# Optimization experiments

Measured on AMD Instinct MI355X. Metric: run time of the kernel, lower is better.

## Reference

```python
import jax, jax.numpy as jnp
import numpy as np

DIM = 2048
N_HEADS = 16
Q_LORA = 1536
KV_LORA = 512
NOPE = 128
ROPE = 64
V_DIM = 128
B, T = 1, 3072
EPS = 1e-6


def rmsnorm(x, w):
    var = jnp.mean(jnp.square(x), axis=-1, keepdims=True)
    return x * jax.lax.rsqrt(var + EPS) * w


def apply_rope(x, cos, sin):
    # x: (B, T, H, d); cos/sin: (T, d//2) -> broadcast (1, T, 1, d//2)
    c = cos[None, :, None, :]
    s = sin[None, :, None, :]
    x1 = x[..., 0::2]
    x2 = x[..., 1::2]
    r1 = x1 * c - x2 * s
    r2 = x1 * s + x2 * c
    return jnp.stack([r1, r2], axis=-1).reshape(x.shape)


def setup_inputs() -> dict:
    key = jax.random.key(0)
    ks = jax.random.split(key, 10)
    std = 0.02
    x = jax.random.normal(ks[0], (B, T, DIM), dtype=jnp.float32)
    # RoPE angles: position * inv_freq, shape (T, ROPE//2)
    inv_freq = 1.0 / (10000.0 ** (np.arange(0, ROPE, 2, dtype=np.float32) / ROPE))
    freqs = jnp.asarray(np.arange(T, dtype=np.float32)[:, None] * inv_freq[None, :])
    # additive causal mask (T, T)
    mask = jnp.where(jnp.tril(jnp.ones((T, T), dtype=bool)), 0.0, -jnp.inf).astype(jnp.float32)
    wq_down = jax.random.normal(ks[1], (DIM, Q_LORA), dtype=jnp.float32) * std
    q_norm_w = jnp.ones((Q_LORA,), dtype=jnp.float32)
    wq_nope = jax.random.normal(ks[2], (Q_LORA, N_HEADS * NOPE), dtype=jnp.float32) * std
    wq_rope = jax.random.normal(ks[3], (Q_LORA, N_HEADS * ROPE), dtype=jnp.float32) * std
    wkv_down = jax.random.normal(ks[4], (DIM, KV_LORA + ROPE), dtype=jnp.float32) * std
    kv_norm_w = jnp.ones((KV_LORA,), dtype=jnp.float32)
    wkv_up = jax.random.normal(ks[5], (KV_LORA, N_HEADS * (NOPE + V_DIM)), dtype=jnp.float32) * std
    wo = jax.random.normal(ks[6], (N_HEADS * V_DIM, DIM), dtype=jnp.float32) * std
    return {
        'x': x, 'freqs': freqs, 'mask': mask,
        'wq_down': wq_down, 'q_norm_w': q_norm_w, 'wq_nope': wq_nope,
        'wq_rope': wq_rope, 'wkv_down': wkv_down, 'kv_norm_w': kv_norm_w,
        'wkv_up': wkv_up, 'wo': wo,
    }


def reference(x, freqs, mask, wq_down, q_norm_w, wq_nope, wq_rope,
              wkv_down, kv_norm_w, wkv_up, wo):
    cos, sin = jnp.cos(freqs), jnp.sin(freqs)
    # Q path: down-project, RMSNorm, split nope/rope heads
    q_lat = rmsnorm(x @ wq_down, q_norm_w)                      # (B,T,Q_LORA)
    q_nope = (q_lat @ wq_nope).reshape(B, T, N_HEADS, NOPE)
    q_rope = apply_rope((q_lat @ wq_rope).reshape(B, T, N_HEADS, ROPE), cos, sin)
    q = jnp.concatenate([q_nope, q_rope], axis=-1)              # (B,T,H,192)
    # KV path: joint down-projection -> latent c_kv + raw rope key
    kvd = x @ wkv_down                                          # (B,T,KV_LORA+ROPE)
    c_kv = kvd[..., :KV_LORA]
    k_rope_raw = kvd[..., KV_LORA:]                             # (B,T,ROPE)
    k_rope = jnp.broadcast_to(k_rope_raw[:, :, None, :], (B, T, N_HEADS, ROPE))
    k_rope = apply_rope(k_rope, cos, sin)
    kv_up = (rmsnorm(c_kv, kv_norm_w) @ wkv_up).reshape(B, T, N_HEADS, NOPE + V_DIM)
    k_nope = kv_up[..., :NOPE]
    v = kv_up[..., NOPE:]                                       # (B,T,H,V_DIM)
    k = jnp.concatenate([k_nope, k_rope], axis=-1)              # (B,T,H,192)
    scale = (NOPE + ROPE) ** (-0.5)
    attn = jnp.einsum('bqhd,bkhd->bhqk', q, k) * scale + mask[None, None]
    attn = jax.nn.softmax(attn, axis=-1)                        # dropout p=0 (eval)
    out = jnp.einsum('bhqk,bkhd->bqhd', attn, v).reshape(B, T, N_HEADS * V_DIM)
    return out @ wo                                             # (B,T,DIM)
```

## Files before the change

kernel.cpp:

```cpp
#include <hip/hip_runtime.h>
#include <hip/hip_bf16.h>

typedef __bf16 bf16_t;
typedef __bf16 bf16x8 __attribute__((ext_vector_type(8)));
typedef float f32x4 __attribute__((ext_vector_type(4)));

#define T_SEQ 3072
#define DIM 2048
#define NH 16
#define QLORA 1536
#define KVLORA 512
#define NOPE 128
#define ROPE 64
#define VDIM 128
#define HD 192
#define SCALE 0.07216878364870323f
#define CHUNK 12

__device__ inline float wave_reduce_sum(float v) {
    #pragma unroll
    for (int off = 32; off > 0; off >>= 1) v += __shfl_down(v, off);
    return v;
}

__device__ inline float block_reduce_sum_256(float v) {
    __shared__ float red[4];
    int lane = threadIdx.x & 63, w = threadIdx.x >> 6;
    v = wave_reduce_sum(v);
    if (lane == 0) red[w] = v;
    __syncthreads();
    if (threadIdx.x == 0) red[0] = red[0] + red[1] + red[2] + red[3];
    __syncthreads();
    return red[0];
}

__device__ inline void glds16(const bf16_t* g, bf16_t* l) {
    __builtin_amdgcn_global_load_lds(
        (const __attribute__((address_space(1))) unsigned int*)g,
        (__attribute__((address_space(3))) unsigned int*)l, 16, 0, 0);
}

__global__ void f2b_kernel(const float* __restrict__ in, bf16_t* __restrict__ out, int n) {
    int i = (blockIdx.x * 256 + threadIdx.x) * 4;
    if (i < n) {
        float4 v = *(const float4*)&in[i];
        bf16_t o[4] = {(bf16_t)v.x, (bf16_t)v.y, (bf16_t)v.z, (bf16_t)v.w};
        *(uint2*)&out[i] = *(const uint2*)o;
    }
}

__global__ __launch_bounds__(256) void transp_kernel(
    const float* __restrict__ in, bf16_t* __restrict__ out, int K, int N)
{
    __shared__ float tile[32][33];
    int k0 = blockIdx.y * 32, n0 = blockIdx.x * 32;
    int tx = threadIdx.x & 31, ty = threadIdx.x >> 5;
    #pragma unroll
    for (int i = 0; i < 4; ++i)
        tile[ty + i * 8][tx] = in[(size_t)(k0 + ty + i * 8) * N + n0 + tx];
    __syncthreads();
    #pragma unroll
    for (int i = 0; i < 4; ++i)
        out[(size_t)(n0 + ty + i * 8) * K + k0 + tx] = (bf16_t)tile[tx][ty + i * 8];
}

__global__ __launch_bounds__(256) void vt_transp(
    const bf16_t* __restrict__ kvu, bf16_t* __restrict__ vt)
{
    __shared__ bf16_t tile[32][34];
    int t0 = blockIdx.x * 32, d0 = blockIdx.y * 32, h = blockIdx.z;
    int tx = threadIdx.x & 31, ty = threadIdx.x >> 5;
    #pragma unroll
    for (int i = 0; i < 4; ++i)
        tile[ty + i * 8][tx] = kvu[(size_t)(t0 + ty + i * 8) * (NH * 256) + h * 256 + NOPE + d0 + tx];
    __syncthreads();
    #pragma unroll
    for (int i = 0; i < 4; ++i)
        vt[((size_t)h * VDIM + d0 + ty + i * 8) * T_SEQ + t0 + tx] = tile[tx][ty + i * 8];
}

__global__ __launch_bounds__(256) void gemm_mfma(
    const bf16_t* __restrict__ A, const bf16_t* __restrict__ Bt,
    float* __restrict__ Cf, bf16_t* __restrict__ Cb,
    int M, int N, int K, int writef)
{
    __shared__ __align__(16) bf16_t As[128 * 32];
    __shared__ __align__(16) bf16_t Bs[128 * 32];
    int tid = threadIdx.x;
    int w = tid >> 6, lane = tid & 63;
    int quad = lane >> 4, l16 = lane & 15;
    int bm = blockIdx.y * 128, bn = blockIdx.x * 128;
    int wm = (w & 1) * 64, wn = (w >> 1) * 64;

    int srow = tid >> 2, soff = (tid & 3) * 8;
    const bf16_t* a0 = A + (size_t)(bm + srow) * K + soff;
    const bf16_t* a1 = A + (size_t)(bm + 64 + srow) * K + soff;
    int br0 = bn + srow;      if (br0 >= N) br0 = N - 1;
    int br1 = bn + 64 + srow; if (br1 >= N) br1 = N - 1;
    const bf16_t* b0 = Bt + (size_t)br0 * K + soff;
    const bf16_t* b1 = Bt + (size_t)br1 * K + soff;
    bf16_t* la = &As[tid * 8];
    bf16_t* lb = &Bs[tid * 8];

    f32x4 acc[4][4];
    #pragma unroll
    for (int i = 0; i < 4; ++i)
        #pragma unroll
        for (int j = 0; j < 4; ++j)
            acc[i][j] = (f32x4){0.f, 0.f, 0.f, 0.f};

    for (int k0 = 0; k0 < K; k0 += 32) {
        glds16(a0 + k0, la);
        glds16(a1 + k0, la + 2048);
        glds16(b0 + k0, lb);
        glds16(b1 + k0, lb + 2048);
        __syncthreads();
        bf16x8 af[4], bfr[4];
        #pragma unroll
        for (int t = 0; t < 4; ++t) {
            af[t]  = *(const bf16x8*)&As[(wm + t * 16 + l16) * 32 + quad * 8];
            bfr[t] = *(const bf16x8*)&Bs[(wn + t * 16 + l16) * 32 + quad * 8];
        }
        #pragma unroll
        for (int i = 0; i < 4; ++i)
            #pragma unroll
            for (int j = 0; j < 4; ++j)
                acc[i][j] = __builtin_amdgcn_mfma_f32_16x16x32_bf16(af[i], bfr[j], acc[i][j], 0, 0, 0);
        __syncthreads();
    }

    #pragma unroll
    for (int i = 0; i < 4; ++i) {
        #pragma unroll
        for (int j = 0; j < 4; ++j) {
            #pragma unroll
            for (int r = 0; r < 4; ++r) {
                int row = bm + wm + i * 16 + quad * 4 + r;
                int col = bn + wn + j * 16 + l16;
                if (col < N) {
                    if (writef) Cf[(size_t)row * N + col] = acc[i][j][r];
                    else        Cb[(size_t)row * N + col] = (bf16_t)acc[i][j][r];
                }
            }
        }
    }
}

__global__ __launch_bounds__(256) void rmsnorm_rows(
    bf16_t* __restrict__ X, const float* __restrict__ w, int N)
{
    int row = blockIdx.x;
    bf16_t* x = X + (size_t)row * N;
    float ss = 0.f;
    for (int i = threadIdx.x; i < N; i += 256) { float v = (float)x[i]; ss += v * v; }
    ss = block_reduce_sum_256(ss);
    float sc = rsqrtf(ss / (float)N + 1e-6f);
    for (int i = threadIdx.x; i < N; i += 256)
        x[i] = (bf16_t)((float)x[i] * sc * w[i]);
}

__global__ __launch_bounds__(256) void kv_post(
    const bf16_t* __restrict__ kvd, const float* __restrict__ w,
    const float* __restrict__ freqs,
    bf16_t* __restrict__ ckvn, bf16_t* __restrict__ kr)
{
    int row = blockIdx.x;
    const bf16_t* src = kvd + (size_t)row * (KVLORA + ROPE);
    float ss = 0.f;
    for (int i = threadIdx.x; i < KVLORA; i += 256) { float v = (float)src[i]; ss += v * v; }
    ss = block_reduce_sum_256(ss);
    float sc = rsqrtf(ss / (float)KVLORA + 1e-6f);
    for (int i = threadIdx.x; i < KVLORA; i += 256)
        ckvn[(size_t)row * KVLORA + i] = (bf16_t)((float)src[i] * sc * w[i]);
    if (threadIdx.x < 32) {
        int i = threadIdx.x;
        float f = freqs[row * 32 + i];
        float c = cosf(f), s = sinf(f);
        float x1 = (float)src[KVLORA + 2 * i], x2 = (float)src[KVLORA + 2 * i + 1];
        kr[(size_t)row * ROPE + 2 * i]     = (bf16_t)(x1 * c - x2 * s);
        kr[(size_t)row * ROPE + 2 * i + 1] = (bf16_t)(x1 * s + x2 * c);
    }
}

__global__ void rope_q(bf16_t* __restrict__ qr, const float* __restrict__ freqs) {
    int idx = blockIdx.x * 256 + threadIdx.x;
    if (idx >= T_SEQ * NH * 32) return;
    int t = idx >> 9;
    int rem = idx & 511;
    int h = rem >> 5;
    int i = rem & 31;
    float f = freqs[t * 32 + i];
    float c = cosf(f), s = sinf(f);
    bf16_t* p = qr + (size_t)t * (NH * ROPE) + h * ROPE + 2 * i;
    float x1 = (float)p[0], x2 = (float)p[1];
    p[0] = (bf16_t)(x1 * c - x2 * s);
    p[1] = (bf16_t)(x1 * s + x2 * c);
}

#define P_STRIDE 72
__device__ inline int slot_base(int qt, int h) {
    int b = qt / CHUNK;
    return h * 120 + qt + 6 * b * (b - 1) + (qt - CHUNK * b) * b;
}
__global__ __launch_bounds__(256) void attn_v8(
    const bf16_t* __restrict__ QN, const bf16_t* __restrict__ QR,
    const bf16_t* __restrict__ KVU, const bf16_t* __restrict__ KR,
    const bf16_t* __restrict__ Vt,
    bf16_t* __restrict__ Opart, float* __restrict__ lpart)
{
    __shared__ __align__(16) bf16_t Kn[64 * 128];
    __shared__ __align__(16) bf16_t Kr[64 * 64];
    __shared__ __align__(16) bf16_t Vs[128 * 64];
    __shared__ __align__(16) bf16_t Ps[4][16 * P_STRIDE];

    int qt = blockIdx.x, cx = blockIdx.y, h = blockIdx.z;
    if (cx > qt / CHUNK) return;
    int slot = slot_base(qt, h) + cx;
    int kt0 = cx * CHUNK;
    int kt1 = min(qt + 1, kt0 + CHUNK);

    int tid = threadIdx.x;
    int w = tid >> 6, lane = tid & 63;
    int quad = lane >> 4, l16 = lane & 15;
    int qbase = qt * 64;

    bf16x8 qf[6];
    {
        int qrow = qbase + w * 16 + l16;
        #pragma unroll
        for (int kk = 0; kk < 4; ++kk)
            qf[kk] = *(const bf16x8*)&QN[(size_t)qrow * (NH * NOPE) + h * NOPE + kk * 32 + quad * 8];
        #pragma unroll
        for (int kk = 4; kk < 6; ++kk)
            qf[kk] = *(const bf16x8*)&QR[(size_t)qrow * (NH * ROPE) + h * ROPE + (kk - 4) * 32 + quad * 8];
    }

    int l4 = lane >> 4, l3 = lane >> 3;
    const bf16_t* kn_e = KVU + (size_t)(kt0 * 64 + w * 16 + l4) * (NH * 256) + h * 256 + ((lane & 15) ^ l4) * 8;
    const bf16_t* kn_o = KVU + (size_t)(kt0 * 64 + w * 16 + l4) * (NH * 256) + h * 256 + ((lane & 15) ^ (4 + l4)) * 8;
    const bf16_t* krp  = KR  + (size_t)(kt0 * 64 + w * 16 + l3) * ROPE + ((lane & 7) ^ l3) * 8;
    const bf16_t* vp   = Vt  + ((size_t)h * VDIM + w * 32 + l3) * T_SEQ + kt0 * 64 + ((lane & 7) ^ l3) * 8;

    bf16x8 ones;
    #pragma unroll
    for (int i = 0; i < 8; ++i) ones[i] = (bf16_t)1.0f;

    f32x4 o[8];
    #pragma unroll
    for (int nt = 0; nt < 8; ++nt) o[nt] = (f32x4){0.f, 0.f, 0.f, 0.f};
    f32x4 lacc = (f32x4){0.f, 0.f, 0.f, 0.f};

    for (int kt = kt0; kt < kt1; ++kt) {
        int kbase = kt * 64;
        #pragma unroll
        for (int i = 0; i < 4; ++i)
            glds16(((i & 1) ? kn_o : kn_e) + (size_t)i * 4 * (NH * 256), &Kn[(w * 4 + i) * 512]);
        #pragma unroll
        for (int i = 0; i < 2; ++i)
            glds16(krp + (size_t)i * 8 * ROPE, &Kr[(w * 2 + i) * 512]);
        #pragma unroll
        for (int i = 0; i < 4; ++i)
            glds16(vp + (size_t)i * 8 * T_SEQ, &Vs[(w * 4 + i) * 512]);
        kn_e += (size_t)64 * NH * 256;
        kn_o += (size_t)64 * NH * 256;
        krp  += 64 * ROPE;
        vp   += 64;
        __syncthreads();

        f32x4 S[4];
        #pragma unroll
        for (int c = 0; c < 4; ++c) S[c] = (f32x4){0.f, 0.f, 0.f, 0.f};
        #pragma unroll
        for (int kk = 0; kk < 4; ++kk) {
            #pragma unroll
            for (int c = 0; c < 4; ++c) {
                bf16x8 kf = *(const bf16x8*)&Kn[(c * 16 + l16) * 128 + (((kk * 4 + quad) ^ (l16 & 7)) * 8)];
                S[c] = __builtin_amdgcn_mfma_f32_16x16x32_bf16(qf[kk], kf, S[c], 0, 0, 0);
            }
        }
        #pragma unroll
        for (int kk = 4; kk < 6; ++kk) {
            #pragma unroll
            for (int c = 0; c < 4; ++c) {
                bf16x8 kf = *(const bf16x8*)&Kr[(c * 16 + l16) * 64 + ((((kk - 4) * 4 + quad) ^ (l16 & 7)) * 8)];
                S[c] = __builtin_amdgcn_mfma_f32_16x16x32_bf16(qf[kk], kf, S[c], 0, 0, 0);
            }
        }

        #pragma unroll
        for (int c = 0; c < 4; ++c) {
            #pragma unroll
            for (int j = 0; j < 4; ++j) {
                int col = kbase + c * 16 + l16;
                int grow = qbase + w * 16 + quad * 4 + j;
                float p = (col <= grow) ? __expf(S[c][j] * SCALE) : 0.f;
                Ps[w][(quad * 4 + j) * P_STRIDE + c * 16 + l16] = (bf16_t)p;
            }
        }
        __asm__ volatile("s_waitcnt lgkmcnt(0)" ::: "memory");

        bf16x8 pf0 = *(const bf16x8*)&Ps[w][l16 * P_STRIDE + quad * 8];
        bf16x8 pf1 = *(const bf16x8*)&Ps[w][l16 * P_STRIDE + 32 + quad * 8];
        lacc = __builtin_amdgcn_mfma_f32_16x16x32_bf16(pf0, ones, lacc, 0, 0, 0);
        lacc = __builtin_amdgcn_mfma_f32_16x16x32_bf16(pf1, ones, lacc, 0, 0, 0);

        #pragma unroll
        for (int kk2 = 0; kk2 < 2; ++kk2) {
            bf16x8 pf = kk2 ? pf1 : pf0;
            #pragma unroll
            for (int nt = 0; nt < 8; ++nt) {
                bf16x8 vf = *(const bf16x8*)&Vs[(nt * 16 + l16) * 64 + (((kk2 * 4 + quad) ^ (l16 & 7)) * 8)];
                o[nt] = __builtin_amdgcn_mfma_f32_16x16x32_bf16(pf, vf, o[nt], 0, 0, 0);
            }
        }
        __syncthreads();
    }

    #pragma unroll
    for (int nt = 0; nt < 8; ++nt)
        #pragma unroll
        for (int j = 0; j < 4; ++j)
            Opart[(size_t)slot * 8192 + (w * 16 + quad * 4 + j) * 128 + nt * 16 + l16] = (bf16_t)o[nt][j];
    if (l16 == 0) {
        #pragma unroll
        for (int j = 0; j < 4; ++j)
            lpart[slot * 64 + w * 16 + quad * 4 + j] = lacc[j];
    }
}

__global__ __launch_bounds__(256) void attn_combine(
    const bf16_t* __restrict__ Opart, const float* __restrict__ lpart,
    bf16_t* __restrict__ AO)
{
    int qt = blockIdx.x, h = blockIdx.y;
    int nch = qt / CHUNK + 1;
    int base = slot_base(qt, h);
    int r = threadIdx.x >> 2, c0 = (threadIdx.x & 3) * 32;

    float acc[32];
    #pragma unroll
    for (int i = 0; i < 32; ++i) acc[i] = 0.f;
    float lsum = 0.f;
    for (int ch = 0; ch < nch; ++ch) {
        int slot = base + ch;
        const bf16_t* p = &Opart[(size_t)slot * 8192 + r * 128 + c0];
        #pragma unroll
        for (int v = 0; v < 4; ++v) {
            bf16x8 u = *(const bf16x8*)&p[v * 8];
            #pragma unroll
            for (int e = 0; e < 8; ++e) acc[v * 8 + e] += (float)u[e];
        }
        lsum += lpart[slot * 64 + r];
    }
    float inv = 1.0f / lsum;
    bf16_t* dst = AO + (size_t)(qt * 64 + r) * (NH * VDIM) + h * VDIM + c0;
    #pragma unroll
    for (int v = 0; v < 4; ++v) {
        bf16_t tmp[8];
        #pragma unroll
        for (int e = 0; e < 8; ++e) tmp[e] = (bf16_t)(acc[v * 8 + e] * inv);
        *(uint4*)&dst[v * 8] = *(const uint4*)tmp;
    }
}

extern "C" void kernel_launch(void* const* d_in, const int* in_sizes, int n_in,
                              void* d_out, int out_size, void* d_ws, size_t ws_size,
                              hipStream_t stream) {
    const float* x        = (const float*)d_in[0];
    const float* freqs    = (const float*)d_in[1];
    const float* wq_down  = (const float*)d_in[3];
    const float* q_norm_w = (const float*)d_in[4];
    const float* wq_nope  = (const float*)d_in[5];
    const float* wq_rope  = (const float*)d_in[6];
    const float* wkv_down = (const float*)d_in[7];
    const float* kv_norm_w= (const float*)d_in[8];
    const float* wkv_up   = (const float*)d_in[9];
    const float* wo       = (const float*)d_in[10];
    float* out = (float*)d_out;

    bf16_t* ws = (bf16_t*)d_ws;
    bf16_t* xb     = ws;
    bf16_t* wqd_t  = xb     + 6291456;
    bf16_t* wkvd_t = wqd_t  + 3145728;
    bf16_t* wqn_t  = wkvd_t + 1179648;
    bf16_t* wqr_t  = wqn_t  + 3145728;
    bf16_t* wkvu_t = wqr_t  + 1572864;
    bf16_t* t1     = wkvu_t + 2097152;
    bf16_t* kvd    = t1     + 4718592;
    bf16_t* ckvn   = kvd    + 1769472;
    bf16_t* Opart  = ws;
    float*  lpart  = (float*)(ws + 15728640);
    bf16_t* ao     = ws + 15728640 + 245760;
    bf16_t* wo_t   = ws    + 25493504;
    bf16_t* kr     = wo_t  + 4194304;
    bf16_t* qn     = kr    + 196608;
    bf16_t* qr     = qn    + 6291456;
    bf16_t* kvu    = qr    + 3145728;
    bf16_t* vt     = kvu   + 12582912;

    f2b_kernel<<<T_SEQ * DIM / 4 / 256, 256, 0, stream>>>(x, xb, T_SEQ * DIM);
    transp_kernel<<<dim3(QLORA / 32, DIM / 32), 256, 0, stream>>>(wq_down, wqd_t, DIM, QLORA);
    transp_kernel<<<dim3((KVLORA + ROPE) / 32, DIM / 32), 256, 0, stream>>>(wkv_down, wkvd_t, DIM, KVLORA + ROPE);
    transp_kernel<<<dim3(NH * NOPE / 32, QLORA / 32), 256, 0, stream>>>(wq_nope, wqn_t, QLORA, NH * NOPE);
    transp_kernel<<<dim3(NH * ROPE / 32, QLORA / 32), 256, 0, stream>>>(wq_rope, wqr_t, QLORA, NH * ROPE);
    transp_kernel<<<dim3(NH * 256 / 32, KVLORA / 32), 256, 0, stream>>>(wkv_up, wkvu_t, KVLORA, NH * 256);
    transp_kernel<<<dim3(DIM / 32, DIM / 32), 256, 0, stream>>>(wo, wo_t, DIM, DIM);

    gemm_mfma<<<dim3(QLORA / 128, T_SEQ / 128), 256, 0, stream>>>(xb, wqd_t, nullptr, t1, T_SEQ, QLORA, DIM, 0);
    gemm_mfma<<<dim3(5, T_SEQ / 128), 256, 0, stream>>>(xb, wkvd_t, nullptr, kvd, T_SEQ, KVLORA + ROPE, DIM, 0);

    rmsnorm_rows<<<T_SEQ, 256, 0, stream>>>(t1, q_norm_w, QLORA);
    kv_post<<<T_SEQ, 256, 0, stream>>>(kvd, kv_norm_w, freqs, ckvn, kr);

    gemm_mfma<<<dim3(NH * NOPE / 128, T_SEQ / 128), 256, 0, stream>>>(t1, wqn_t, nullptr, qn, T_SEQ, NH * NOPE, QLORA, 0);
    gemm_mfma<<<dim3(NH * ROPE / 128, T_SEQ / 128), 256, 0, stream>>>(t1, wqr_t, nullptr, qr, T_SEQ, NH * ROPE, QLORA, 0);
    rope_q<<<(T_SEQ * NH * 32 + 255) / 256, 256, 0, stream>>>(qr, freqs);
    gemm_mfma<<<dim3(NH * 256 / 128, T_SEQ / 128), 256, 0, stream>>>(ckvn, wkvu_t, nullptr, kvu, T_SEQ, NH * 256, KVLORA, 0);

    vt_transp<<<dim3(T_SEQ / 32, VDIM / 32, NH), 256, 0, stream>>>(kvu, vt);

    attn_v8<<<dim3(T_SEQ / 64, 4, NH), 256, 0, stream>>>(qn, qr, kvu, kr, vt, Opart, lpart);
    attn_combine<<<dim3(T_SEQ / 64, NH), 256, 0, stream>>>(Opart, lpart, ao);

    gemm_mfma<<<dim3(DIM / 128, T_SEQ / 128), 256, 0, stream>>>(ao, wo_t, out, nullptr, T_SEQ, DIM, DIM, 1);
}
```

Before: 572.5 us.

## Double-buffer GEMM LDS loads and merge sibling projection GEMMs

```diff
diff --git a/kernel.cpp b/kernel.cpp
--- a/kernel.cpp
+++ b/kernel.cpp
@@ -17,6 +17,9 @@
 #define SCALE 0.07216878364870323f
 #define CHUNK 12
 
+#define T1KV_LD 2112
+#define QNR_LD 3072
+
 __device__ inline float wave_reduce_sum(float v) {
     #pragma unroll
     for (int off = 32; off > 0; off >>= 1) v += __shfl_down(v, off);
@@ -82,10 +85,10 @@
 __global__ __launch_bounds__(256) void gemm_mfma(
     const bf16_t* __restrict__ A, const bf16_t* __restrict__ Bt,
     float* __restrict__ Cf, bf16_t* __restrict__ Cb,
-    int M, int N, int K, int writef)
-{
-    __shared__ __align__(16) bf16_t As[128 * 32];
-    __shared__ __align__(16) bf16_t Bs[128 * 32];
+    int M, int N, int K, int lda, int ldb, int ldc, int writef)
+{
+    __shared__ __align__(16) bf16_t As[2][128 * 32];
+    __shared__ __align__(16) bf16_t Bs[2][128 * 32];
     int tid = threadIdx.x;
     int w = tid >> 6, lane = tid & 63;
     int quad = lane >> 4, l16 = lane & 15;
@@ -93,14 +96,12 @@
     int wm = (w & 1) * 64, wn = (w >> 1) * 64;
 
     int srow = tid >> 2, soff = (tid & 3) * 8;
-    const bf16_t* a0 = A + (size_t)(bm + srow) * K + soff;
-    const bf16_t* a1 = A + (size_t)(bm + 64 + srow) * K + soff;
+    const bf16_t* a0 = A + (size_t)(bm + srow) * lda + soff;
+    const bf16_t* a1 = A + (size_t)(bm + 64 + srow) * lda + soff;
     int br0 = bn + srow;      if (br0 >= N) br0 = N - 1;
     int br1 = bn + 64 + srow; if (br1 >= N) br1 = N - 1;
-    const bf16_t* b0 = Bt + (size_t)br0 * K + soff;
-    const bf16_t* b1 = Bt + (size_t)br1 * K + soff;
-    bf16_t* la = &As[tid * 8];
-    bf16_t* lb = &Bs[tid * 8];
+    const bf16_t* b0 = Bt + (size_t)br0 * ldb + soff;
+    const bf16_t* b1 = Bt + (size_t)br1 * ldb + soff;
 
     f32x4 acc[4][4];
     #pragma unroll
@@ -109,24 +110,43 @@
         for (int j = 0; j < 4; ++j)
             acc[i][j] = (f32x4){0.f, 0.f, 0.f, 0.f};
 
-    for (int k0 = 0; k0 < K; k0 += 32) {
-        glds16(a0 + k0, la);
-        glds16(a1 + k0, la + 2048);
-        glds16(b0 + k0, lb);
-        glds16(b1 + k0, lb + 2048);
-        __syncthreads();
+    int nk = K >> 5;
+    glds16(a0, &As[0][tid * 8]);
+    glds16(a1, &As[0][tid * 8 + 2048]);
+    glds16(b0, &Bs[0][tid * 8]);
+    glds16(b1, &Bs[0][tid * 8 + 2048]);
+    a0 += 32; a1 += 32; b0 += 32; b1 += 32;
+
+    for (int t = 0; t < nk; ++t) {
+        int cur = t & 1;
+        if (t + 1 < nk) {
+            int nxt = cur ^ 1;
+            glds16(a0, &As[nxt][tid * 8]);
+            glds16(a1, &As[nxt][tid * 8 + 2048]);
+            glds16(b0, &Bs[nxt][tid * 8]);
+            glds16(b1, &Bs[nxt][tid * 8 + 2048]);
+            a0 += 32; a1 += 32; b0 += 32; b1 += 32;
+            asm volatile("s_waitcnt vmcnt(4)" ::: "memory");
+        } else {
+            asm volatile("s_waitcnt vmcnt(0)" ::: "memory");
+        }
+        __builtin_amdgcn_s_barrier();
+        __builtin_amdgcn_sched_barrier(0);
+
         bf16x8 af[4], bfr[4];
         #pragma unroll
-        for (int t = 0; t < 4; ++t) {
-            af[t]  = *(const bf16x8*)&As[(wm + t * 16 + l16) * 32 + quad * 8];
-            bfr[t] = *(const bf16x8*)&Bs[(wn + t * 16 + l16) * 32 + quad * 8];
+        for (int t4 = 0; t4 < 4; ++t4) {
+            af[t4]  = *(const bf16x8*)&As[cur][(wm + t4 * 16 + l16) * 32 + quad * 8];
+            bfr[t4] = *(const bf16x8*)&Bs[cur][(wn + t4 * 16 + l16) * 32 + quad * 8];
         }
         #pragma unroll
         for (int i = 0; i < 4; ++i)
             #pragma unroll
             for (int j = 0; j < 4; ++j)
                 acc[i][j] = __builtin_amdgcn_mfma_f32_16x16x32_bf16(af[i], bfr[j], acc[i][j], 0, 0, 0);
-        __syncthreads();
+
+        __builtin_amdgcn_sched_barrier(0);
+        __builtin_amdgcn_s_barrier();
     }
 
     #pragma unroll
@@ -138,8 +158,8 @@
                 int row = bm + wm + i * 16 + quad * 4 + r;
                 int col = bn + wn + j * 16 + l16;
                 if (col < N) {
-                    if (writef) Cf[(size_t)row * N + col] = acc[i][j][r];
-                    else        Cb[(size_t)row * N + col] = (bf16_t)acc[i][j][r];
+                    if (writef) Cf[(size_t)row * ldc + col] = acc[i][j][r];
+                    else        Cb[(size_t)row * ldc + col] = (bf16_t)acc[i][j][r];
                 }
             }
         }
@@ -147,10 +167,10 @@
 }
 
 __global__ __launch_bounds__(256) void rmsnorm_rows(
-    bf16_t* __restrict__ X, const float* __restrict__ w, int N)
+    bf16_t* __restrict__ X, const float* __restrict__ w, int N, int ld)
 {
     int row = blockIdx.x;
-    bf16_t* x = X + (size_t)row * N;
+    bf16_t* x = X + (size_t)row * ld;
     float ss = 0.f;
     for (int i = threadIdx.x; i < N; i += 256) { float v = (float)x[i]; ss += v * v; }
     ss = block_reduce_sum_256(ss);
@@ -165,7 +185,7 @@
     bf16_t* __restrict__ ckvn, bf16_t* __restrict__ kr)
 {
     int row = blockIdx.x;
-    const bf16_t* src = kvd + (size_t)row * (KVLORA + ROPE);
+    const bf16_t* src = kvd + (size_t)row * T1KV_LD;
     float ss = 0.f;
     for (int i = threadIdx.x; i < KVLORA; i += 256) { float v = (float)src[i]; ss += v * v; }
     ss = block_reduce_sum_256(ss);
@@ -191,7 +211,7 @@
     int i = rem & 31;
     float f = freqs[t * 32 + i];
     float c = cosf(f), s = sinf(f);
-    bf16_t* p = qr + (size_t)t * (NH * ROPE) + h * ROPE + 2 * i;
+    bf16_t* p = qr + (size_t)t * QNR_LD + h * ROPE + 2 * i;
     float x1 = (float)p[0], x2 = (float)p[1];
     p[0] = (bf16_t)(x1 * c - x2 * s);
     p[1] = (bf16_t)(x1 * s + x2 * c);
@@ -203,7 +223,7 @@
     return h * 120 + qt + 6 * b * (b - 1) + (qt - CHUNK * b) * b;
 }
 __global__ __launch_bounds__(256) void attn_v8(
-    const bf16_t* __restrict__ QN, const bf16_t* __restrict__ QR,
+    const bf16_t* __restrict__ QNR,
     const bf16_t* __restrict__ KVU, const bf16_t* __restrict__ KR,
     const bf16_t* __restrict__ Vt,
     bf16_t* __restrict__ Opart, float* __restrict__ lpart)
@@ -229,10 +249,10 @@
         int qrow = qbase + w * 16 + l16;
         #pragma unroll
         for (int kk = 0; kk < 4; ++kk)
-            qf[kk] = *(const bf16x8*)&QN[(size_t)qrow * (NH * NOPE) + h * NOPE + kk * 32 + quad * 8];
+            qf[kk] = *(const bf16x8*)&QNR[(size_t)qrow * QNR_LD + h * NOPE + kk * 32 + quad * 8];
         #pragma unroll
         for (int kk = 4; kk < 6; ++kk)
-            qf[kk] = *(const bf16x8*)&QR[(size_t)qrow * (NH * ROPE) + h * ROPE + (kk - 4) * 32 + quad * 8];
+            qf[kk] = *(const bf16x8*)&QNR[(size_t)qrow * QNR_LD + (NH * NOPE) + h * ROPE + (kk - 4) * 32 + quad * 8];
     }
 
     int l4 = lane >> 4, l3 = lane >> 3;
@@ -385,17 +405,15 @@
     bf16_t* wqn_t  = wkvd_t + 1179648;
     bf16_t* wqr_t  = wqn_t  + 3145728;
     bf16_t* wkvu_t = wqr_t  + 1572864;
-    bf16_t* t1     = wkvu_t + 2097152;
-    bf16_t* kvd    = t1     + 4718592;
-    bf16_t* ckvn   = kvd    + 1769472;
+    bf16_t* t1kv   = wkvu_t + 2097152;
+    bf16_t* ckvn   = t1kv   + 6488064;
     bf16_t* Opart  = ws;
     float*  lpart  = (float*)(ws + 15728640);
     bf16_t* ao     = ws + 15728640 + 245760;
     bf16_t* wo_t   = ws    + 25493504;
     bf16_t* kr     = wo_t  + 4194304;
-    bf16_t* qn     = kr    + 196608;
-    bf16_t* qr     = qn    + 6291456;
-    bf16_t* kvu    = qr    + 3145728;
+    bf16_t* qnr    = kr    + 196608;
+    bf16_t* kvu    = qnr   + 9437184;
     bf16_t* vt     = kvu   + 12582912;
 
     f2b_kernel<<<T_SEQ * DIM / 4 / 256, 256, 0, stream>>>(x, xb, T_SEQ * DIM);
@@ -406,21 +424,24 @@
     transp_kernel<<<dim3(NH * 256 / 32, KVLORA / 32), 256, 0, stream>>>(wkv_up, wkvu_t, KVLORA, NH * 256);
     transp_kernel<<<dim3(DIM / 32, DIM / 32), 256, 0, stream>>>(wo, wo_t, DIM, DIM);
 
-    gemm_mfma<<<dim3(QLORA / 128, T_SEQ / 128), 256, 0, stream>>>(xb, wqd_t, nullptr, t1, T_SEQ, QLORA, DIM, 0);
-    gemm_mfma<<<dim3(5, T_SEQ / 128), 256, 0, stream>>>(xb, wkvd_t, nullptr, kvd, T_SEQ, KVLORA + ROPE, DIM, 0);
-
-    rmsnorm_rows<<<T_SEQ, 256, 0, stream>>>(t1, q_norm_w, QLORA);
-    kv_post<<<T_SEQ, 256, 0, stream>>>(kvd, kv_norm_w, freqs, ckvn, kr);
-
-    gemm_mfma<<<dim3(NH * NOPE / 128, T_SEQ / 128), 256, 0, stream>>>(t1, wqn_t, nullptr, qn, T_SEQ, NH * NOPE, QLORA, 0);
-    gemm_mfma<<<dim3(NH * ROPE / 128, T_SEQ / 128), 256, 0, stream>>>(t1, wqr_t, nullptr, qr, T_SEQ, NH * ROPE, QLORA, 0);
-    rope_q<<<(T_SEQ * NH * 32 + 255) / 256, 256, 0, stream>>>(qr, freqs);
-    gemm_mfma<<<dim3(NH * 256 / 128, T_SEQ / 128), 256, 0, stream>>>(ckvn, wkvu_t, nullptr, kvu, T_SEQ, NH * 256, KVLORA, 0);
+    gemm_mfma<<<dim3(17, T_SEQ / 128), 256, 0, stream>>>(
+        xb, wqd_t, nullptr, t1kv, T_SEQ, 2112, DIM, DIM, DIM, T1KV_LD, 0);
+
+    rmsnorm_rows<<<T_SEQ, 256, 0, stream>>>(t1kv, q_norm_w, QLORA, T1KV_LD);
+    kv_post<<<T_SEQ, 256, 0, stream>>>(t1kv + QLORA, kv_norm_w, freqs, ckvn, kr);
+
+    gemm_mfma<<<dim3(24, T_SEQ / 128), 256, 0, stream>>>(
+        t1kv, wqn_t, nullptr, qnr, T_SEQ, 3072, QLORA, T1KV_LD, QLORA, QNR_LD, 0);
+    rope_q<<<(T_SEQ * NH * 32 + 255) / 256, 256, 0, stream>>>(qnr + NH * NOPE, freqs);
+
+    gemm_mfma<<<dim3(NH * 256 / 128, T_SEQ / 128), 256, 0, stream>>>(
+        ckvn, wkvu_t, nullptr, kvu, T_SEQ, NH * 256, KVLORA, KVLORA, KVLORA, NH * 256, 0);
 
     vt_transp<<<dim3(T_SEQ / 32, VDIM / 32, NH), 256, 0, stream>>>(kvu, vt);
 
-    attn_v8<<<dim3(T_SEQ / 64, 4, NH), 256, 0, stream>>>(qn, qr, kvu, kr, vt, Opart, lpart);
+    attn_v8<<<dim3(T_SEQ / 64, 4, NH), 256, 0, stream>>>(qnr, kvu, kr, vt, Opart, lpart);
     attn_combine<<<dim3(T_SEQ / 64, NH), 256, 0, stream>>>(Opart, lpart, ao);
 
-    gemm_mfma<<<dim3(DIM / 128, T_SEQ / 128), 256, 0, stream>>>(ao, wo_t, out, nullptr, T_SEQ, DIM, DIM, 1);
-}
+    gemm_mfma<<<dim3(DIM / 128, T_SEQ / 128), 256, 0, stream>>>(
+        ao, wo_t, out, nullptr, T_SEQ, DIM, DIM, DIM, DIM, DIM, 1);
+}
```

After: 476.8 us. 16.7% less time.
